# Optimization experiments

Hardware: AMD Instinct MI355X
Metric: run time of the kernel (lower is better)

## Reference

```python
import jax, jax.numpy as jnp
import numpy as np

IN_FEATURES = 4096
OUT_FEATURES = 4096
BATCH, SEQ = 8, 2048


def setup_inputs() -> dict:
    key = jax.random.key(0)
    k_in, k_w, k_b = jax.random.split(key, 3)
    inputs = {
        "input": jax.random.normal(k_in, (BATCH, SEQ, IN_FEATURES), dtype=jnp.float32),
        # int8-valued weights stored as int32 (range [-128, 127])
        "quantized_weight": jax.random.randint(k_w, (OUT_FEATURES, IN_FEATURES), -128, 128, dtype=jnp.int32),
        "weight_scale": jnp.array([0.01], dtype=jnp.float32),
        "weight_zero_point": jnp.array([2], dtype=jnp.int32),
        # int16-valued bias stored as int32 (range [-32768, 32767])
        "quantized_bias": jax.random.randint(k_b, (OUT_FEATURES,), -32768, 32768, dtype=jnp.int32),
        "bias_scale": jnp.array([0.0005], dtype=jnp.float32),
        "bias_zero_point": jnp.array([1], dtype=jnp.int32),
    }
    return inputs


def reference(input, quantized_weight, weight_scale, weight_zero_point,
              quantized_bias, bias_scale, bias_zero_point) -> jnp.ndarray:
    # Dequantize weights: (q - zp) * scale  -> [out, in] fp32
    w = (quantized_weight.astype(jnp.float32) - weight_zero_point.astype(jnp.float32)) * weight_scale
    # Dequantize bias -> [out] fp32
    b = (quantized_bias.astype(jnp.float32) - bias_zero_point.astype(jnp.float32)) * bias_scale
    # F.linear: input @ w.T + b ; input [B, S, in] -> out [B, S, out]
    return jnp.einsum('bsi,oi->bso', input, w) + b
```

## Files before the change

### kernel.cpp

```cpp
#include <hip/hip_runtime.h>

#define M_DIM 16384
#define N_DIM 4096
#define K_DIM 4096
#define BK 64
#define NKT (K_DIM / BK)

typedef unsigned char u8;
typedef __attribute__((ext_vector_type(4))) int   i32x4;

#define AS1 __attribute__((address_space(1)))
#define AS3 __attribute__((address_space(3)))

__global__ __launch_bounds__(256)
void quant_a_kernel(const float* __restrict__ in, char* __restrict__ out,
                    float* __restrict__ srow, int* __restrict__ rsum) {
    const int row  = blockIdx.x;
    const int t    = threadIdx.x;
    const int lane = t & 63, wv = t >> 6;
    const float4* rp = (const float4*)(in + (size_t)row * K_DIM);

    float4 v[4];
#pragma unroll
    for (int j = 0; j < 4; ++j) v[j] = rp[t + 256 * j];

    float amax = 0.f;
#pragma unroll
    for (int j = 0; j < 4; ++j) {
        amax = fmaxf(amax, fmaxf(fmaxf(fabsf(v[j].x), fabsf(v[j].y)),
                                 fmaxf(fabsf(v[j].z), fabsf(v[j].w))));
    }
#pragma unroll
    for (int off = 32; off; off >>= 1) amax = fmaxf(amax, __shfl_xor(amax, off));
    __shared__ float wred[4];
    __shared__ int   sred[4];
    if (lane == 0) wred[wv] = amax;
    __syncthreads();
    amax = fmaxf(fmaxf(wred[0], wred[1]), fmaxf(wred[2], wred[3]));
    const float inv = amax > 0.f ? 127.f / amax : 0.f;

    int lsum = 0;
    unsigned* orow = (unsigned*)(out + (size_t)row * K_DIM);
#pragma unroll
    for (int j = 0; j < 4; ++j) {
        int q0 = __float2int_rn(v[j].x * inv);
        int q1 = __float2int_rn(v[j].y * inv);
        int q2 = __float2int_rn(v[j].z * inv);
        int q3 = __float2int_rn(v[j].w * inv);
        lsum += q0 + q1 + q2 + q3;
        unsigned pk = (unsigned)(q0 & 0xFF) | ((unsigned)(q1 & 0xFF) << 8) |
                      ((unsigned)(q2 & 0xFF) << 16) | ((unsigned)(q3 & 0xFF) << 24);
        orow[t + 256 * j] = pk;
    }
#pragma unroll
    for (int off = 32; off; off >>= 1) lsum += __shfl_xor(lsum, off);
    if (lane == 0) sred[wv] = lsum;
    __syncthreads();
    if (t == 0) {
        rsum[row] = sred[0] + sred[1] + sred[2] + sred[3];
        srow[row] = amax > 0.f ? amax / 127.f : 1.f;
    }
}

__global__ __launch_bounds__(256)
void pack_w_kernel(const int* __restrict__ q, char* __restrict__ out, int n4) {
    int stride = gridDim.x * blockDim.x;
    for (int i = blockIdx.x * blockDim.x + threadIdx.x; i < n4; i += stride) {
        int4 a = ((const int4*)q)[i];
        unsigned pk = (unsigned)(a.x & 0xFF) | ((unsigned)(a.y & 0xFF) << 8) |
                      ((unsigned)(a.z & 0xFF) << 16) | ((unsigned)(a.w & 0xFF) << 24);
        ((unsigned*)out)[i] = pk;
    }
}

__global__ __launch_bounds__(512, 2)
void gemm_i8_kernel(const char* __restrict__ A, const char* __restrict__ B,
                    const float* __restrict__ srow, const int* __restrict__ rsum,
                    const float* __restrict__ wsc_p, const int* __restrict__ wzp_p,
                    const int* __restrict__ qb, const float* __restrict__ bsc_p,
                    const int* __restrict__ bzp_p, float* __restrict__ C) {
    __shared__ __align__(16) u8 lds[4 * 32768];

    const int nwg = gridDim.x;
    const int cpx = nwg >> 3;
    const int bid = blockIdx.x;
    const int swz = (bid & 7) * cpx + (bid >> 3);
    const int st = swz >> 5, wi = swz & 31;
    const int bm = (st >> 2) * 8 + (wi >> 2);
    const int bn = (st & 3) * 4 + (wi & 3);
    const int m0 = bm * 256, n0 = bn * 256;

    const int tid  = threadIdx.x;
    const int wv   = tid >> 6;
    const int lane = tid & 63;
    const int wr   = wv >> 2;
    const int wcn  = wv & 3;
    const int l15  = lane & 15;

    const int koff = (((lane >> 4) ^ ((lane >> 1) & 3)) << 4);

    const int srt  = tid >> 2;
    const int gcol = (((tid & 3) ^ ((tid >> 3) & 3)) << 4);
    const char* AgT = A + (size_t)(m0 + srt) * K_DIM + gcol;
    const char* BgT = B + (size_t)(n0 + srt) * K_DIM + gcol;
    const int wvo = wv << 10;

    i32x4 acc[8][4] = {};

    auto STAGE_A = [&](int ns, int k3) {
#pragma unroll
        for (int i = 0; i < 2; ++i)
            __builtin_amdgcn_global_load_lds(
                (const AS1 void*)(AgT + (size_t)i * 128 * K_DIM + k3),
                (AS3 void*)(lds + ns * 32768 + i * 8192 + wvo), 16, 0, 0);
    };
    auto STAGE_B = [&](int ns, int k3) {
#pragma unroll
        for (int i = 0; i < 2; ++i)
            __builtin_amdgcn_global_load_lds(
                (const AS1 void*)(BgT + (size_t)i * 128 * K_DIM + k3),
                (AS3 void*)(lds + ns * 32768 + 16384 + i * 8192 + wvo), 16, 0, 0);
    };

    STAGE_A(0, 0);      STAGE_B(0, 0);
    STAGE_A(1, BK);     STAGE_B(1, BK);
    STAGE_A(2, 2 * BK); STAGE_B(2, 2 * BK);
    asm volatile("s_waitcnt vmcnt(8)" ::: "memory");
    __builtin_amdgcn_s_barrier();
    __builtin_amdgcn_sched_barrier(0);

#pragma unroll 2
    for (int u = 0; u < NKT; ++u) {
        const int cs = u & 3;
        const u8* Asl = lds + cs * 32768;
        const u8* Bsl = Asl + 16384;
        const bool pf = (u + 3) < NKT;
        const int ns = (u + 3) & 3;
        const int k3 = (u + 3) * BK;

        i32x4 af[8], bfr[4];

#pragma unroll
        for (int ni = 0; ni < 4; ++ni) {
            int row = wcn * 64 + ni * 16 + l15;
            bfr[ni] = *(const i32x4*)(Bsl + row * 64 + koff);
        }
#pragma unroll
        for (int mi = 0; mi < 8; ++mi) {
            int row = wr * 128 + mi * 16 + l15;
            af[mi] = *(const i32x4*)(Asl + row * 64 + koff);
        }
        if (pf) { STAGE_A(ns, k3); STAGE_B(ns, k3); }

        __builtin_amdgcn_s_setprio(1);
#pragma unroll
        for (int mi = 0; mi < 8; ++mi)
#pragma unroll
            for (int ni = 0; ni < 4; ++ni)
                acc[mi][ni] = __builtin_amdgcn_mfma_i32_16x16x64_i8(
                    af[mi], bfr[ni], acc[mi][ni], 0, 0, 0);
        __builtin_amdgcn_s_setprio(0);

        asm volatile("s_waitcnt lgkmcnt(0)" ::: "memory");
        if (u < NKT - 3)       asm volatile("s_waitcnt vmcnt(8)" ::: "memory");
        else if (u == NKT - 3) asm volatile("s_waitcnt vmcnt(4)" ::: "memory");
        else if (u == NKT - 2) asm volatile("s_waitcnt vmcnt(0)" ::: "memory");
        __builtin_amdgcn_s_barrier();
        __builtin_amdgcn_sched_barrier(0);
    }

    const float ws  = wsc_p[0];
    const float zpf = (float)wzp_p[0];
    const float bsc = bsc_p[0];
    const float bzp = (float)bzp_p[0];
    float bias_[4];
#pragma unroll
    for (int ni = 0; ni < 4; ++ni) {
        int col = n0 + wcn * 64 + ni * 16 + l15;
        bias_[ni] = ((float)qb[col] - bzp) * bsc;
    }
#pragma unroll
    for (int mi = 0; mi < 8; ++mi) {
        int rbase = m0 + wr * 128 + mi * 16 + (lane >> 4) * 4;
        float fs_[4], fc_[4];
#pragma unroll
        for (int i = 0; i < 4; ++i) {
            float sf = ws * srow[rbase + i];
            fs_[i] = sf;
            fc_[i] = -sf * zpf * (float)rsum[rbase + i];
        }
#pragma unroll
        for (int ni = 0; ni < 4; ++ni) {
            int col = n0 + wcn * 64 + ni * 16 + l15;
#pragma unroll
            for (int i = 0; i < 4; ++i)
                C[(size_t)(rbase + i) * N_DIM + col] =
                    fs_[i] * (float)acc[mi][ni][i] + fc_[i] + bias_[ni];
        }
    }
}

__global__ void gemm_fallback_kernel(const float* __restrict__ A, const int* __restrict__ Wq,
                                     const float* __restrict__ wsc_p, const int* __restrict__ wzp_p,
                                     const int* __restrict__ qb, const float* __restrict__ bsc_p,
                                     const int* __restrict__ bzp_p, float* __restrict__ C) {
    int m = blockIdx.y;
    int n = blockIdx.x * 256 + threadIdx.x;
    float zp = (float)wzp_p[0];
    float sc = wsc_p[0];
    __shared__ float Arow[512];
    float acc = 0.f;
    for (int k0 = 0; k0 < K_DIM; k0 += 512) {
        __syncthreads();
        for (int t = threadIdx.x; t < 512; t += 256)
            Arow[t] = A[(size_t)m * K_DIM + k0 + t];
        __syncthreads();
        const int4* wp = (const int4*)(Wq + (size_t)n * K_DIM + k0);
        for (int kk = 0; kk < 512; kk += 4) {
            int4 q = wp[kk >> 2];
            acc += Arow[kk]     * ((float)q.x - zp);
            acc += Arow[kk + 1] * ((float)q.y - zp);
            acc += Arow[kk + 2] * ((float)q.z - zp);
            acc += Arow[kk + 3] * ((float)q.w - zp);
        }
    }
    acc *= sc;
    acc += ((float)qb[n] - (float)bzp_p[0]) * bsc_p[0];
    C[(size_t)m * N_DIM + n] = acc;
}

extern "C" void kernel_launch(void* const* d_in, const int* in_sizes, int n_in,
                              void* d_out, int out_size, void* d_ws, size_t ws_size,
                              hipStream_t stream) {
    (void)in_sizes; (void)n_in; (void)out_size;
    const float* input = (const float*)d_in[0];
    const int*   qw    = (const int*)d_in[1];
    const float* wsc   = (const float*)d_in[2];
    const int*   wzp   = (const int*)d_in[3];
    const int*   qb    = (const int*)d_in[4];
    const float* bsc   = (const float*)d_in[5];
    const int*   bzp   = (const int*)d_in[6];
    float* out = (float*)d_out;

    size_t offA = 0;
    size_t offW = (size_t)M_DIM * K_DIM;
    size_t offS = offW + (size_t)N_DIM * K_DIM;
    size_t offR = offS + (size_t)M_DIM * sizeof(float);
    size_t need = offR + (size_t)M_DIM * sizeof(int);

    if (ws_size >= need) {
        char*  Aq = (char*)d_ws + offA;
        char*  Wq8 = (char*)d_ws + offW;
        float* S  = (float*)((char*)d_ws + offS);
        int*   R  = (int*)((char*)d_ws + offR);
        quant_a_kernel<<<M_DIM, 256, 0, stream>>>(input, Aq, S, R);
        pack_w_kernel<<<2048, 256, 0, stream>>>(qw, Wq8, N_DIM * K_DIM / 4);
        gemm_i8_kernel<<<(M_DIM / 256) * (N_DIM / 256), 512, 0, stream>>>(
            Aq, Wq8, S, R, wsc, wzp, qb, bsc, bzp, out);
    } else {
        dim3 grid(N_DIM / 256, M_DIM);
        gemm_fallback_kernel<<<grid, 256, 0, stream>>>(input, qw, wsc, wzp, qb, bsc, bzp, out);
    }
}
```

Baseline: 379.0 us.

## Shrink GEMM tile to 128x256 and load A fragments directly from global

The int8 GEMM workgroup shrinks from 512 to 256 threads and its tile from 256x256 to 128x256. Only the B (weight) tile is still staged through LDS with async global-to-LDS loads. Each wave now reads its A fragments straight from global memory into registers, and all four waves share the same 128 rows. This cuts LDS use and LDS traffic for A, but adds redundant global/L2 reads of A, exposes global load latency without prefetch, and the vmcnt wait counts may no longer match the reduced number of staged loads.

```diff
diff --git a/kernel.cpp b/kernel.cpp
--- a/kernel.cpp
+++ b/kernel.cpp
@@ -73,13 +73,13 @@
     }
 }
 
-__global__ __launch_bounds__(512, 2)
+__global__ __launch_bounds__(256, 2)
 void gemm_i8_kernel(const char* __restrict__ A, const char* __restrict__ B,
                     const float* __restrict__ srow, const int* __restrict__ rsum,
                     const float* __restrict__ wsc_p, const int* __restrict__ wzp_p,
                     const int* __restrict__ qb, const float* __restrict__ bsc_p,
                     const int* __restrict__ bzp_p, float* __restrict__ C) {
-    __shared__ __align__(16) u8 lds[4 * 32768];
+    __shared__ __align__(16) u8 ldsB[4 * 16384];
 
     const int nwg = gridDim.x;
     const int cpx = nwg >> 3;
@@ -88,69 +88,54 @@
     const int st = swz >> 5, wi = swz & 31;
     const int bm = (st >> 2) * 8 + (wi >> 2);
     const int bn = (st & 3) * 4 + (wi & 3);
-    const int m0 = bm * 256, n0 = bn * 256;
+    const int m0 = bm * 128, n0 = bn * 256;
 
     const int tid  = threadIdx.x;
     const int wv   = tid >> 6;
     const int lane = tid & 63;
-    const int wr   = wv >> 2;
-    const int wcn  = wv & 3;
     const int l15  = lane & 15;
 
     const int koff = (((lane >> 4) ^ ((lane >> 1) & 3)) << 4);
 
-    const int srt  = tid >> 2;
-    const int gcol = (((tid & 3) ^ ((tid >> 3) & 3)) << 4);
-    const char* AgT = A + (size_t)(m0 + srt) * K_DIM + gcol;
-    const char* BgT = B + (size_t)(n0 + srt) * K_DIM + gcol;
+    const int srow_ = wv * 16 + (lane >> 2);
+    const int gcol  = (((lane & 3) ^ ((lane >> 3) & 3)) << 4);
+    const char* BgT = B + (size_t)(n0 + srow_) * K_DIM + gcol;
     const int wvo = wv << 10;
 
+    const char* Ag = A + (size_t)(m0 + l15) * K_DIM + ((lane >> 4) << 4);
+
     i32x4 acc[8][4] = {};
 
-    auto STAGE_A = [&](int ns, int k3) {
-#pragma unroll
-        for (int i = 0; i < 2; ++i)
+    auto STAGE_B = [&](int ns, int k3) {
+#pragma unroll
+        for (int i = 0; i < 4; ++i)
             __builtin_amdgcn_global_load_lds(
-                (const AS1 void*)(AgT + (size_t)i * 128 * K_DIM + k3),
-                (AS3 void*)(lds + ns * 32768 + i * 8192 + wvo), 16, 0, 0);
+                (const AS1 void*)(BgT + (size_t)i * 64 * K_DIM + k3),
+                (AS3 void*)(ldsB + ns * 16384 + i * 4096 + wvo), 16, 0, 0);
     };
-    auto STAGE_B = [&](int ns, int k3) {
-#pragma unroll
-        for (int i = 0; i < 2; ++i)
-            __builtin_amdgcn_global_load_lds(
-                (const AS1 void*)(BgT + (size_t)i * 128 * K_DIM + k3),
-                (AS3 void*)(lds + ns * 32768 + 16384 + i * 8192 + wvo), 16, 0, 0);
-    };
-
-    STAGE_A(0, 0);      STAGE_B(0, 0);
-    STAGE_A(1, BK);     STAGE_B(1, BK);
-    STAGE_A(2, 2 * BK); STAGE_B(2, 2 * BK);
+
+    STAGE_B(0, 0);
+    STAGE_B(1, BK);
+    STAGE_B(2, 2 * BK);
     asm volatile("s_waitcnt vmcnt(8)" ::: "memory");
     __builtin_amdgcn_s_barrier();
     __builtin_amdgcn_sched_barrier(0);
 
-#pragma unroll 2
     for (int u = 0; u < NKT; ++u) {
-        const int cs = u & 3;
-        const u8* Asl = lds + cs * 32768;
-        const u8* Bsl = Asl + 16384;
-        const bool pf = (u + 3) < NKT;
-        const int ns = (u + 3) & 3;
-        const int k3 = (u + 3) * BK;
-
-        i32x4 af[8], bfr[4];
-
-#pragma unroll
-        for (int ni = 0; ni < 4; ++ni) {
-            int row = wcn * 64 + ni * 16 + l15;
-            bfr[ni] = *(const i32x4*)(Bsl + row * 64 + koff);
-        }
-#pragma unroll
-        for (int mi = 0; mi < 8; ++mi) {
-            int row = wr * 128 + mi * 16 + l15;
-            af[mi] = *(const i32x4*)(Asl + row * 64 + koff);
-        }
-        if (pf) { STAGE_A(ns, k3); STAGE_B(ns, k3); }
+        const u8* Bsl = ldsB + (u & 3) * 16384;
+        const int k0 = u * BK;
+
+        i32x4 af[8];
+#pragma unroll
+        for (int mi = 0; mi < 8; ++mi)
+            af[mi] = *(const i32x4*)(Ag + (size_t)(mi * 16) * K_DIM + k0);
+
+        i32x4 bfr[4];
+#pragma unroll
+        for (int ni = 0; ni < 4; ++ni)
+            bfr[ni] = *(const i32x4*)(Bsl + (wv * 64 + ni * 16 + l15) * 64 + koff);
+
+        if (u + 3 < NKT) STAGE_B((u + 3) & 3, (u + 3) * BK);
 
         __builtin_amdgcn_s_setprio(1);
 #pragma unroll
@@ -176,12 +161,12 @@
     float bias_[4];
 #pragma unroll
     for (int ni = 0; ni < 4; ++ni) {
-        int col = n0 + wcn * 64 + ni * 16 + l15;
+        int col = n0 + wv * 64 + ni * 16 + l15;
         bias_[ni] = ((float)qb[col] - bzp) * bsc;
     }
 #pragma unroll
     for (int mi = 0; mi < 8; ++mi) {
-        int rbase = m0 + wr * 128 + mi * 16 + (lane >> 4) * 4;
+        int rbase = m0 + mi * 16 + (lane >> 4) * 4;
         float fs_[4], fc_[4];
 #pragma unroll
         for (int i = 0; i < 4; ++i) {
@@ -191,7 +176,7 @@
         }
 #pragma unroll
         for (int ni = 0; ni < 4; ++ni) {
-            int col = n0 + wcn * 64 + ni * 16 + l15;
+            int col = n0 + wv * 64 + ni * 16 + l15;
 #pragma unroll
             for (int i = 0; i < 4; ++i)
                 C[(size_t)(rbase + i) * N_DIM + col] =
@@ -255,7 +240,7 @@
         int*   R  = (int*)((char*)d_ws + offR);
         quant_a_kernel<<<M_DIM, 256, 0, stream>>>(input, Aq, S, R);
         pack_w_kernel<<<2048, 256, 0, stream>>>(qw, Wq8, N_DIM * K_DIM / 4);
-        gemm_i8_kernel<<<(M_DIM / 256) * (N_DIM / 256), 512, 0, stream>>>(
+        gemm_i8_kernel<<<(M_DIM / 128) * (N_DIM / 256), 256, 0, stream>>>(
             Aq, Wq8, S, R, wsc, wzp, qb, bsc, bzp, out);
     } else {
         dim3 grid(N_DIM / 256, M_DIM);
```

Measured after the change: 665.5 us. 1.76x slower.
